# Optimization experiments

Hardware: AMD Instinct MI355X
Metric: run time of the kernel (lower is better)

The kernel has to match this reference:

```python
import jax, jax.numpy as jnp
import numpy as np

VOCAB, EMB, CLASSES = 100000, 256, 100
B, S, L = 64, 128, 64


def setup_inputs() -> dict:
    key = jax.random.key(0)
    k1, k2, k3, k4, k5 = jax.random.split(key, 5)
    return {
        "tok_lists_batch": jax.random.randint(k1, (B, S, L), 0, VOCAB, dtype=jnp.int64)
        if jax.config.jax_enable_x64 else jax.random.randint(k1, (B, S, L), 0, VOCAB, dtype=jnp.int32),
        "emb_weight": jax.random.normal(k2, (VOCAB, EMB), dtype=jnp.float32),
        "class_embs": jax.random.normal(k3, (CLASSES, EMB), dtype=jnp.float32),
        "multi_weight": jax.random.normal(k4, (CLASSES, EMB), dtype=jnp.float32),
        "multi_bias": jax.random.normal(k5, (CLASSES, 1), dtype=jnp.float32),
    }


def reference(tok_lists_batch, emb_weight, class_embs, multi_weight, multi_bias):
    # EmbeddingBag(mode='mean'): gather token embeddings then mean over sent_len.
    # sents: (B, S, E)
    sents = jnp.mean(emb_weight[tok_lists_batch], axis=2)
    # attention scores: (B, C, S) = class_embs @ sents^T, softmax over sentences
    scores = jnp.einsum("ce,bse->bcs", class_embs, sents)
    atts = jax.nn.softmax(scores, axis=-1)
    # mixes: (B, C, E)
    mixes = jnp.einsum("bcs,bse->bce", atts, sents)
    # per-class linear: logits[b,c] = mixes[b,c,:] . multi_weight[c,:] + bias[c]
    logits = jnp.einsum("bce,ce->bc", mixes, multi_weight) + multi_bias[:, 0][None, :]
    return logits
```

## Files before the change

### kernel.cpp

```cpp
#include <hip/hip_runtime.h>

#define EMB  256
#define NCLS 100
#define NB   64
#define NS   128
#define NL   64
#define CCH  10

__global__ __launch_bounds__(256) void k_gather_mean(
    const int* __restrict__ tok, const float* __restrict__ emb,
    float* __restrict__ sents)
{
    const int sid = blockIdx.x;
    const int tid = threadIdx.x;
    __shared__ int   toks[NL];
    __shared__ float part[4][EMB];

    if (tid < NL) toks[tid] = tok[(size_t)sid * NL + tid];
    __syncthreads();

    const int g    = tid >> 6;
    const int lane = tid & 63;

    float4 acc = make_float4(0.f, 0.f, 0.f, 0.f);
    #pragma unroll
    for (int i = 0; i < NL / 4; ++i) {
        const int l = g + (i << 2);
        const float4* row = reinterpret_cast<const float4*>(emb + (size_t)toks[l] * EMB);
        float4 v = row[lane];
        acc.x += v.x; acc.y += v.y; acc.z += v.z; acc.w += v.w;
    }
    reinterpret_cast<float4*>(&part[g][0])[lane] = acc;
    __syncthreads();

    const float ssum = part[0][tid] + part[1][tid] + part[2][tid] + part[3][tid];
    sents[(size_t)sid * EMB + tid] = ssum * (1.0f / NL);
}

__global__ __launch_bounds__(128) void k_attn_logits(
    const float* __restrict__ sents, const float* __restrict__ ce,
    const float* __restrict__ mw,    const float* __restrict__ bias,
    float* __restrict__ out)
{
    const int b  = blockIdx.x;
    const int c0 = blockIdx.y * CCH;
    const int s  = threadIdx.x;

    __shared__ float ce_l[CCH][EMB];
    __shared__ float mw_l[CCH][EMB];
    __shared__ float sc_l[CCH][NS];
    __shared__ float tv_l[CCH][NS];

    for (int i = s; i < CCH * EMB; i += 128) {
        const int c = i >> 8, e = i & (EMB - 1);
        ce_l[c][e] = ce[(size_t)(c0 + c) * EMB + e];
        mw_l[c][e] = mw[(size_t)(c0 + c) * EMB + e];
    }
    __syncthreads();

    float sc[CCH], tv[CCH];
    #pragma unroll
    for (int c = 0; c < CCH; ++c) { sc[c] = 0.f; tv[c] = 0.f; }

    const float* row = sents + ((size_t)b * NS + s) * EMB;
    for (int eb = 0; eb < EMB; eb += 64) {
        float4 r[16];
        #pragma unroll
        for (int i = 0; i < 16; ++i)
            r[i] = reinterpret_cast<const float4*>(row + eb)[i];
        #pragma unroll
        for (int c = 0; c < CCH; ++c) {
            float a = 0.f, t = 0.f;
            #pragma unroll
            for (int i = 0; i < 16; ++i) {
                const int e = eb + (i << 2);
                a += r[i].x * ce_l[c][e]     + r[i].y * ce_l[c][e + 1]
                   + r[i].z * ce_l[c][e + 2] + r[i].w * ce_l[c][e + 3];
                t += r[i].x * mw_l[c][e]     + r[i].y * mw_l[c][e + 1]
                   + r[i].z * mw_l[c][e + 2] + r[i].w * mw_l[c][e + 3];
            }
            sc[c] += a; tv[c] += t;
        }
    }

    #pragma unroll
    for (int c = 0; c < CCH; ++c) { sc_l[c][s] = sc[c]; tv_l[c][s] = tv[c]; }
    __syncthreads();

    const int wid = s >> 6, lane = s & 63;
    for (int c = wid; c < CCH; c += 2) {
        const float x0 = sc_l[c][lane], x1 = sc_l[c][lane + 64];
        float m = fmaxf(x0, x1);
        #pragma unroll
        for (int d = 1; d < 64; d <<= 1) m = fmaxf(m, __shfl_xor(m, d));
        const float p0 = __expf(x0 - m), p1 = __expf(x1 - m);
        const float t0 = tv_l[c][lane],  t1 = tv_l[c][lane + 64];
        float sp = p0 + p1;
        float st = p0 * t0 + p1 * t1;
        #pragma unroll
        for (int d = 1; d < 64; d <<= 1) {
            sp += __shfl_xor(sp, d);
            st += __shfl_xor(st, d);
        }
        if (lane == 0)
            out[(size_t)b * NCLS + c0 + c] = st / sp + bias[c0 + c];
    }
}

extern "C" void kernel_launch(void* const* d_in, const int* in_sizes, int n_in,
                              void* d_out, int out_size, void* d_ws, size_t ws_size,
                              hipStream_t stream)
{
    const int*   tok  = (const int*)  d_in[0];
    const float* emb  = (const float*)d_in[1];
    const float* ce   = (const float*)d_in[2];
    const float* mw   = (const float*)d_in[3];
    const float* bias = (const float*)d_in[4];
    float* out   = (float*)d_out;
    float* sents = (float*)d_ws;

    k_gather_mean<<<NB * NS, 256, 0, stream>>>(tok, emb, sents);
    k_attn_logits<<<dim3(NB, NCLS / CCH), 128, 0, stream>>>(sents, ce, mw, bias, out);
}
```

Baseline: 250.5 us.

## Restructure gather to wave-per-sentence and register-tile attention over sentences and classes

The gather kernel now gives each wavefront a whole sentence. It broadcasts token ids with readlane and batches eight row loads before accumulating, which drops the LDS partial reduction and the block barriers. The attention kernel now has each thread compute 4 sentences by 2 classes from float4 weights in padded shared memory, with 20 classes per block. This raises data reuse per load and cuts redundant reads of the sentence rows. The cost is more registers per thread and fewer blocks in the second kernel.

```diff
diff --git a/kernel.cpp b/kernel.cpp
--- a/kernel.cpp
+++ b/kernel.cpp
@@ -1,100 +1,118 @@
 #include <hip/hip_runtime.h>
 
-#define EMB  256
-#define NCLS 100
-#define NB   64
-#define NS   128
-#define NL   64
-#define CCH  10
+#define EMB   256
+#define NCLS  100
+#define NB    64
+#define NS    128
+#define NL    64
+#define CB    20
+#define K2T   320
 
 __global__ __launch_bounds__(256) void k_gather_mean(
     const int* __restrict__ tok, const float* __restrict__ emb,
     float* __restrict__ sents)
 {
-    const int sid = blockIdx.x;
-    const int tid = threadIdx.x;
-    __shared__ int   toks[NL];
-    __shared__ float part[4][EMB];
+    const int w    = threadIdx.x >> 6;
+    const int lane = threadIdx.x & 63;
+    const int sid  = blockIdx.x * 4 + w;
 
-    if (tid < NL) toks[tid] = tok[(size_t)sid * NL + tid];
-    __syncthreads();
-
-    const int g    = tid >> 6;
-    const int lane = tid & 63;
+    const int mytok = tok[(size_t)sid * NL + lane];
 
     float4 acc = make_float4(0.f, 0.f, 0.f, 0.f);
-    #pragma unroll
-    for (int i = 0; i < NL / 4; ++i) {
-        const int l = g + (i << 2);
-        const float4* row = reinterpret_cast<const float4*>(emb + (size_t)toks[l] * EMB);
-        float4 v = row[lane];
-        acc.x += v.x; acc.y += v.y; acc.z += v.z; acc.w += v.w;
+    for (int i = 0; i < NL; i += 8) {
+        float4 v[8];
+        #pragma unroll
+        for (int j = 0; j < 8; ++j) {
+            const int tk = __builtin_amdgcn_readlane(mytok, i + j);
+            v[j] = reinterpret_cast<const float4*>(emb + (size_t)tk * EMB)[lane];
+        }
+        #pragma unroll
+        for (int j = 0; j < 8; ++j) {
+            acc.x += v[j].x; acc.y += v[j].y; acc.z += v[j].z; acc.w += v[j].w;
+        }
     }
-    reinterpret_cast<float4*>(&part[g][0])[lane] = acc;
-    __syncthreads();
-
-    const float ssum = part[0][tid] + part[1][tid] + part[2][tid] + part[3][tid];
-    sents[(size_t)sid * EMB + tid] = ssum * (1.0f / NL);
+    const float s = 1.0f / NL;
+    float4 r; r.x = acc.x * s; r.y = acc.y * s; r.z = acc.z * s; r.w = acc.w * s;
+    reinterpret_cast<float4*>(sents + (size_t)sid * EMB)[lane] = r;
 }
 
-__global__ __launch_bounds__(128) void k_attn_logits(
+__device__ __forceinline__ float dot4(float4 a, float4 b) {
+    return a.x * b.x + a.y * b.y + a.z * b.z + a.w * b.w;
+}
+
+__global__ __launch_bounds__(K2T, 2) void k_attn_logits(
     const float* __restrict__ sents, const float* __restrict__ ce,
     const float* __restrict__ mw,    const float* __restrict__ bias,
     float* __restrict__ out)
 {
     const int b  = blockIdx.x;
-    const int c0 = blockIdx.y * CCH;
-    const int s  = threadIdx.x;
+    const int c0 = blockIdx.y * CB;
+    const int t  = threadIdx.x;
+    const int sg = t & 31;
+    const int cq = t >> 5;
 
-    __shared__ float ce_l[CCH][EMB];
-    __shared__ float mw_l[CCH][EMB];
-    __shared__ float sc_l[CCH][NS];
-    __shared__ float tv_l[CCH][NS];
+    __shared__ float4 wgt[CB][2][66];
+    __shared__ float  red[CB][2][NS];
 
-    for (int i = s; i < CCH * EMB; i += 128) {
-        const int c = i >> 8, e = i & (EMB - 1);
-        ce_l[c][e] = ce[(size_t)(c0 + c) * EMB + e];
-        mw_l[c][e] = mw[(size_t)(c0 + c) * EMB + e];
+    for (int i = t; i < CB * 2 * 64; i += K2T) {
+        const int c  = i >> 7;
+        const int a  = (i >> 6) & 1;
+        const int e4 = i & 63;
+        const float* src = a ? mw : ce;
+        wgt[c][a][e4] =
+            reinterpret_cast<const float4*>(src + (size_t)(c0 + c) * EMB)[e4];
     }
     __syncthreads();
 
-    float sc[CCH], tv[CCH];
+    float scA[4], tvA[4], scB[4], tvB[4];
     #pragma unroll
-    for (int c = 0; c < CCH; ++c) { sc[c] = 0.f; tv[c] = 0.f; }
+    for (int j = 0; j < 4; ++j) { scA[j] = tvA[j] = scB[j] = tvB[j] = 0.f; }
 
-    const float* row = sents + ((size_t)b * NS + s) * EMB;
-    for (int eb = 0; eb < EMB; eb += 64) {
-        float4 r[16];
+    const int cA = 2 * cq, cB = 2 * cq + 1;
+    const float* srow = sents + ((size_t)b * NS + sg * 4) * EMB;
+
+    for (int e8 = 0; e8 < EMB / 8; ++e8) {
+        float4 sv[4][2];
         #pragma unroll
-        for (int i = 0; i < 16; ++i)
-            r[i] = reinterpret_cast<const float4*>(row + eb)[i];
+        for (int j = 0; j < 4; ++j) {
+            const float4* rp =
+                reinterpret_cast<const float4*>(srow + (size_t)j * EMB) + e8 * 2;
+            sv[j][0] = rp[0];
+            sv[j][1] = rp[1];
+        }
+        const float4 wA0 = wgt[cA][0][e8 * 2], wA1 = wgt[cA][0][e8 * 2 + 1];
+        const float4 mA0 = wgt[cA][1][e8 * 2], mA1 = wgt[cA][1][e8 * 2 + 1];
+        const float4 wB0 = wgt[cB][0][e8 * 2], wB1 = wgt[cB][0][e8 * 2 + 1];
+        const float4 mB0 = wgt[cB][1][e8 * 2], mB1 = wgt[cB][1][e8 * 2 + 1];
         #pragma unroll
-        for (int c = 0; c < CCH; ++c) {
-            float a = 0.f, t = 0.f;
-            #pragma unroll
-            for (int i = 0; i < 16; ++i) {
-                const int e = eb + (i << 2);
-                a += r[i].x * ce_l[c][e]     + r[i].y * ce_l[c][e + 1]
-                   + r[i].z * ce_l[c][e + 2] + r[i].w * ce_l[c][e + 3];
-                t += r[i].x * mw_l[c][e]     + r[i].y * mw_l[c][e + 1]
-                   + r[i].z * mw_l[c][e + 2] + r[i].w * mw_l[c][e + 3];
-            }
-            sc[c] += a; tv[c] += t;
+        for (int j = 0; j < 4; ++j) {
+            scA[j] += dot4(sv[j][0], wA0) + dot4(sv[j][1], wA1);
+            tvA[j] += dot4(sv[j][0], mA0) + dot4(sv[j][1], mA1);
+            scB[j] += dot4(sv[j][0], wB0) + dot4(sv[j][1], wB1);
+            tvB[j] += dot4(sv[j][0], mB0) + dot4(sv[j][1], mB1);
         }
     }
 
     #pragma unroll
-    for (int c = 0; c < CCH; ++c) { sc_l[c][s] = sc[c]; tv_l[c][s] = tv[c]; }
+    for (int j = 0; j < 4; ++j) {
+        red[cA][0][sg * 4 + j] = scA[j];
+        red[cA][1][sg * 4 + j] = tvA[j];
+        red[cB][0][sg * 4 + j] = scB[j];
+        red[cB][1][sg * 4 + j] = tvB[j];
+    }
     __syncthreads();
 
-    const int wid = s >> 6, lane = s & 63;
-    for (int c = wid; c < CCH; c += 2) {
-        const float x0 = sc_l[c][lane], x1 = sc_l[c][lane + 64];
+    const int wv   = t >> 6;
+    const int lane = t & 63;
+    #pragma unroll
+    for (int k = 0; k < 4; ++k) {
+        const int cl = wv * 4 + k;
+        const float x0 = red[cl][0][lane], x1 = red[cl][0][lane + 64];
         float m = fmaxf(x0, x1);
         #pragma unroll
         for (int d = 1; d < 64; d <<= 1) m = fmaxf(m, __shfl_xor(m, d));
         const float p0 = __expf(x0 - m), p1 = __expf(x1 - m);
-        const float t0 = tv_l[c][lane],  t1 = tv_l[c][lane + 64];
+        const float t0 = red[cl][1][lane], t1 = red[cl][1][lane + 64];
         float sp = p0 + p1;
         float st = p0 * t0 + p1 * t1;
         #pragma unroll
@@ -103,7 +121,7 @@
             st += __shfl_xor(st, d);
         }
         if (lane == 0)
-            out[(size_t)b * NCLS + c0 + c] = st / sp + bias[c0 + c];
+            out[(size_t)b * NCLS + c0 + cl] = st / sp + bias[c0 + cl];
     }
 }
 
@@ -119,6 +137,6 @@
     float* out   = (float*)d_out;
     float* sents = (float*)d_ws;
 
-    k_gather_mean<<<NB * NS, 256, 0, stream>>>(tok, emb, sents);
-    k_attn_logits<<<dim3(NB, NCLS / CCH), 128, 0, stream>>>(sents, ce, mw, bias, out);
+    k_gather_mean<<<NB * NS / 4, 256, 0, stream>>>(tok, emb, sents);
+    k_attn_logits<<<dim3(NB, NCLS / CB), K2T, 0, stream>>>(sents, ce, mw, bias, out);
 }
```

Result: slower. 286.1 us (+14.2%).
